# Performance work log

Measured on AMD Instinct MI355X. Metric: run time of the kernel, lower is better.

The kernel has to match this reference:

```python
import jax, jax.numpy as jnp
import numpy as np

# Problem sizes: batch(+heads), seq (m=n), head dim, nonzeros per row
B, M, N, K, R = 8, 4096, 4096, 64, 128
NNZ = M * R


def setup_inputs() -> dict:
    key = jax.random.key(0)
    k1, k2, k3, k4 = jax.random.split(key, 4)
    # Uniform CSR: R nonzeros per row, columns sorted within each row.
    row_offsets = jnp.arange(M + 1, dtype=jnp.int32) * R
    column_indices = jax.random.randint(k4, (M, R), 0, N, dtype=jnp.int32)
    column_indices = jnp.sort(column_indices, axis=1).reshape(NNZ)
    # diffsort(row_offsets): row ids sorted by descending row length (load balancing,
    # does not affect the math).
    diffs = row_offsets[1:] - row_offsets[:-1]
    row_indices = jnp.argsort(-diffs).astype(jnp.int32)
    q3d = jax.random.normal(k1, (B, M, K), dtype=jnp.float32)
    k3d = jax.random.normal(k2, (B, N, K), dtype=jnp.float32)
    v3d = jax.random.normal(k3, (B, N, K), dtype=jnp.float32)
    # `values` is only an output buffer for sddmm in the original; contents unused.
    values = jnp.zeros((B, NNZ), dtype=jnp.float32)
    return {
        "row_indices": row_indices,
        "row_offsets": row_offsets,
        "column_indices": column_indices,
        "q3d": q3d,
        "k3d": k3d,
        "v3d": v3d,
        "values": values,
    }


def reference(row_indices, row_offsets, column_indices, q3d, k3d, v3d, values):
    m = row_offsets.shape[0] - 1
    nnz = column_indices.shape[0]
    # Row id of each CSR nonzero.
    row_ids = jnp.searchsorted(
        row_offsets, jnp.arange(nnz, dtype=row_offsets.dtype), side="right"
    ) - 1
    cols = column_indices

    # SDDMM: logits[b, e] = <Q[b, row(e), :], K[b, col(e), :]>  -> [B, nnz]
    logits = jnp.einsum("bed,bed->be", q3d[:, row_ids, :], k3d[:, cols, :])

    def attend_one(lg_b, v_b):
        # Sparse per-row softmax over the nonzeros of each row.
        mx = jax.ops.segment_max(lg_b, row_ids, num_segments=m)
        ex = jnp.exp(lg_b - mx[row_ids])
        den = jax.ops.segment_sum(ex, row_ids, num_segments=m)
        w = ex / den[row_ids]  # [nnz]
        # SPMM: out[i, :] = sum_{e in row i} w[e] * V[col(e), :]
        return jax.ops.segment_sum(w[:, None] * v_b[cols, :], row_ids, num_segments=m)

    return jax.vmap(attend_one)(logits, v3d)  # [B, M, K]
```

## Files before the change

kernel.cpp:

```cpp
#include <hip/hip_runtime.h>

#define Bc 8
#define Mc 4096
#define Nc 4096
#define Kc 64
#define Rc 128

typedef _Float16 h16;
typedef h16 h16x2 __attribute__((ext_vector_type(2)));
typedef h16 h16x4 __attribute__((ext_vector_type(4)));
typedef h16 h16x8 __attribute__((ext_vector_type(8)));
typedef float f32x4 __attribute__((ext_vector_type(4)));

__global__ __launch_bounds__(256) void cvt_fp16(
    const f32x4* __restrict__ K4, const f32x4* __restrict__ V4,
    const f32x4* __restrict__ Q4,
    h16x4* __restrict__ Kh4, h16x4* __restrict__ Vh4, h16x4* __restrict__ Qh4)
{
    const int nb4   = Nc * Kc / 4;
    const int b     = blockIdx.x & 7;
    const int chunk = blockIdx.x >> 3;
    const int tsel  = chunk >> 8;
    const int idx   = b * nb4 + ((chunk & 255) << 8) + threadIdx.x;
    const f32x4* src = (tsel == 0) ? K4 : (tsel == 1) ? V4 : Q4;
    h16x4*       dst = (tsel == 0) ? Kh4 : (tsel == 1) ? Vh4 : Qh4;
    f32x4 v = __builtin_nontemporal_load(&src[idx]);
    h16x4 o = { (h16)v.x, (h16)v.y, (h16)v.z, (h16)v.w };
    dst[idx] = o;
}

__global__ __launch_bounds__(256, 4) void sattn_kernel(
    const int* __restrict__ cols,
    const h16* __restrict__ Qh,
    const h16* __restrict__ Kh,
    const h16* __restrict__ Vh,
    float* __restrict__ out)
{
    const int b   = blockIdx.x & 7;
    const int w   = threadIdx.x >> 6;
    const int row = ((blockIdx.x >> 3) << 2) | w;
    const int l   = threadIdx.x & 63;
    const int g   = l >> 3;
    const int ln  = l & 7;

    const h16* Kb = Kh + ((size_t)b * Nc) * Kc;
    const h16* Vb = Vh + ((size_t)b * Nc) * Kc;

    h16x8 qv = __builtin_nontemporal_load(
        (const h16x8*)(Qh + (((size_t)b * Mc + row) << 6) + ln * 8));

    const int* crow = cols + row * Rc;
    int col16[16];
    #pragma unroll
    for (int p = 0; p < 16; ++p)
        col16[p] = __builtin_nontemporal_load(&crow[p * 8 + g]);

    h16x8 kv[16];
    #pragma unroll
    for (int p = 0; p < 16; ++p)
        kv[p] = *(const h16x8*)(Kb + (((unsigned)col16[p]) << 6) + ln * 8);

    float lg[16];
    #pragma unroll
    for (int p = 0; p < 16; ++p) {
        float acc = 0.f;
        #pragma unroll
        for (int j = 0; j < 4; ++j) {
            h16x2 qj = { qv[2 * j], qv[2 * j + 1] };
            h16x2 kj = { kv[p][2 * j], kv[p][2 * j + 1] };
#if defined(__has_builtin)
#if __has_builtin(__builtin_amdgcn_fdot2)
            acc = __builtin_amdgcn_fdot2(qj, kj, acc, false);
#else
            acc += (float)qj.x * (float)kj.x + (float)qj.y * (float)kj.y;
#endif
#else
            acc += (float)qj.x * (float)kj.x + (float)qj.y * (float)kj.y;
#endif
        }
        acc += __shfl_xor(acc, 1, 64);
        acc += __shfl_xor(acc, 2, 64);
        acc += __shfl_xor(acc, 4, 64);
        lg[p] = acc;
    }

    h16x8 vv[16];
    #pragma unroll
    for (int p = 0; p < 16; ++p)
        vv[p] = *(const h16x8*)(Vb + (((unsigned)col16[p]) << 6) + ln * 8);

    float m = lg[0];
    #pragma unroll
    for (int p = 1; p < 16; ++p) m = fmaxf(m, lg[p]);
    m = fmaxf(m, __shfl_xor(m, 8, 64));
    m = fmaxf(m, __shfl_xor(m, 16, 64));
    m = fmaxf(m, __shfl_xor(m, 32, 64));

    float e[16];
    float s = 0.f;
    #pragma unroll
    for (int p = 0; p < 16; ++p) { e[p] = __expf(lg[p] - m); s += e[p]; }
    s += __shfl_xor(s, 8, 64);
    s += __shfl_xor(s, 16, 64);
    s += __shfl_xor(s, 32, 64);
    const float inv = 1.0f / s;

    float acc8[8] = {0.f, 0.f, 0.f, 0.f, 0.f, 0.f, 0.f, 0.f};
    #pragma unroll
    for (int p = 0; p < 16; ++p) {
        const float wp = e[p];
        #pragma unroll
        for (int j = 0; j < 8; ++j)
            acc8[j] = fmaf((float)vv[p][j], wp, acc8[j]);
    }

    #pragma unroll
    for (int j = 0; j < 8; ++j) {
        acc8[j] += __shfl_xor(acc8[j], 8, 64);
        acc8[j] += __shfl_xor(acc8[j], 16, 64);
        acc8[j] += __shfl_xor(acc8[j], 32, 64);
    }

    if (g == 0) {
        float* orow = out + (((size_t)b * Mc + row) << 6) + ln * 8;
        f32x4 o0 = { acc8[0] * inv, acc8[1] * inv, acc8[2] * inv, acc8[3] * inv };
        f32x4 o1 = { acc8[4] * inv, acc8[5] * inv, acc8[6] * inv, acc8[7] * inv };
        __builtin_nontemporal_store(o0, (f32x4*)orow);
        __builtin_nontemporal_store(o1, (f32x4*)orow + 1);
    }
}

extern "C" void kernel_launch(void* const* d_in, const int* in_sizes, int n_in,
                              void* d_out, int out_size, void* d_ws, size_t ws_size,
                              hipStream_t stream) {
    const int*   cols = (const int*)d_in[2];
    const float* Qm   = (const float*)d_in[3];
    const float* Km   = (const float*)d_in[4];
    const float* Vm   = (const float*)d_in[5];
    float* out = (float*)d_out;

    h16* Kh = (h16*)d_ws;
    h16* Vh = Kh + (size_t)Bc * Nc * Kc;
    h16* Qh = Vh + (size_t)Bc * Nc * Kc;

    cvt_fp16<<<dim3(Bc * 3 * 256), dim3(256), 0, stream>>>(
        (const f32x4*)Km, (const f32x4*)Vm, (const f32x4*)Qm,
        (h16x4*)Kh, (h16x4*)Vh, (h16x4*)Qh);

    sattn_kernel<<<dim3(Bc * Mc / 4), dim3(256), 0, stream>>>(cols, Qh, Kh, Vh, out);
}
```

Baseline: 154.1 us.

## Split each row's nonzeros across two wavefronts with shared-memory softmax merge

Result: faster. 144.7 us (-6.1%).

```diff
diff --git a/kernel.cpp b/kernel.cpp
--- a/kernel.cpp
+++ b/kernel.cpp
@@ -29,40 +29,45 @@
     dst[idx] = o;
 }
 
-__global__ __launch_bounds__(256, 4) void sattn_kernel(
+__global__ __launch_bounds__(256, 6) void sattn_kernel(
     const int* __restrict__ cols,
     const h16* __restrict__ Qh,
     const h16* __restrict__ Kh,
     const h16* __restrict__ Vh,
     float* __restrict__ out)
 {
-    const int b   = blockIdx.x & 7;
-    const int w   = threadIdx.x >> 6;
-    const int row = ((blockIdx.x >> 3) << 2) | w;
-    const int l   = threadIdx.x & 63;
-    const int g   = l >> 3;
-    const int ln  = l & 7;
+    const int b    = blockIdx.x & 7;
+    const int rb   = blockIdx.x >> 3;
+    const int w    = threadIdx.x >> 6;
+    const int rw   = w >> 1;
+    const int half = w & 1;
+    const int row  = rb * 2 + rw;
+    const int l    = threadIdx.x & 63;
+    const int g    = l >> 3;
+    const int ln   = l & 7;
+
+    __shared__ float s_m[2][2];
+    __shared__ float s_s[2][2];
+    __shared__ __align__(16) float s_part[2][64];
 
     const h16* Kb = Kh + ((size_t)b * Nc) * Kc;
     const h16* Vb = Vh + ((size_t)b * Nc) * Kc;
 
-    h16x8 qv = __builtin_nontemporal_load(
-        (const h16x8*)(Qh + (((size_t)b * Mc + row) << 6) + ln * 8));
+    h16x8 qv = *(const h16x8*)(Qh + (((size_t)b * Mc + row) << 6) + ln * 8);
 
-    const int* crow = cols + row * Rc;
-    int col16[16];
+    const int* crow = cols + row * Rc + half * 64;
+    int col8[8];
     #pragma unroll
-    for (int p = 0; p < 16; ++p)
-        col16[p] = __builtin_nontemporal_load(&crow[p * 8 + g]);
+    for (int p = 0; p < 8; ++p) col8[p] = crow[p * 8 + g];
 
-    h16x8 kv[16];
+    h16x8 kv[8];
     #pragma unroll
-    for (int p = 0; p < 16; ++p)
-        kv[p] = *(const h16x8*)(Kb + (((unsigned)col16[p]) << 6) + ln * 8);
+    for (int p = 0; p < 8; ++p)
+        kv[p] = *(const h16x8*)(Kb + (((unsigned)col8[p]) << 6) + ln * 8);
 
-    float lg[16];
+    float lg[8];
     #pragma unroll
-    for (int p = 0; p < 16; ++p) {
+    for (int p = 0; p < 8; ++p) {
         float acc = 0.f;
         #pragma unroll
         for (int j = 0; j < 4; ++j) {
@@ -84,36 +89,37 @@
         lg[p] = acc;
     }
 
-    h16x8 vv[16];
+    h16x8 vv[8];
     #pragma unroll
-    for (int p = 0; p < 16; ++p)
-        vv[p] = *(const h16x8*)(Vb + (((unsigned)col16[p]) << 6) + ln * 8);
+    for (int p = 0; p < 8; ++p)
+        vv[p] = *(const h16x8*)(Vb + (((unsigned)col8[p]) << 6) + ln * 8);
 
     float m = lg[0];
     #pragma unroll
-    for (int p = 1; p < 16; ++p) m = fmaxf(m, lg[p]);
+    for (int p = 1; p < 8; ++p) m = fmaxf(m, lg[p]);
     m = fmaxf(m, __shfl_xor(m, 8, 64));
     m = fmaxf(m, __shfl_xor(m, 16, 64));
     m = fmaxf(m, __shfl_xor(m, 32, 64));
+    if (l == 0) s_m[rw][half] = m;
+    __syncthreads();
+    m = fmaxf(s_m[rw][0], s_m[rw][1]);
 
-    float e[16];
     float s = 0.f;
     #pragma unroll
-    for (int p = 0; p < 16; ++p) { e[p] = __expf(lg[p] - m); s += e[p]; }
+    for (int p = 0; p < 8; ++p) { lg[p] = __expf(lg[p] - m); s += lg[p]; }
     s += __shfl_xor(s, 8, 64);
     s += __shfl_xor(s, 16, 64);
     s += __shfl_xor(s, 32, 64);
-    const float inv = 1.0f / s;
+    if (l == 0) s_s[rw][half] = s;
 
     float acc8[8] = {0.f, 0.f, 0.f, 0.f, 0.f, 0.f, 0.f, 0.f};
     #pragma unroll
-    for (int p = 0; p < 16; ++p) {
-        const float wp = e[p];
+    for (int p = 0; p < 8; ++p) {
+        const float wp = lg[p];
         #pragma unroll
         for (int j = 0; j < 8; ++j)
             acc8[j] = fmaf((float)vv[p][j], wp, acc8[j]);
     }
-
     #pragma unroll
     for (int j = 0; j < 8; ++j) {
         acc8[j] += __shfl_xor(acc8[j], 8, 64);
@@ -121,10 +127,20 @@
         acc8[j] += __shfl_xor(acc8[j], 32, 64);
     }
 
-    if (g == 0) {
+    if (half == 1 && g == 0) {
+        *(f32x4*)&s_part[rw][ln * 8]     = f32x4{acc8[0], acc8[1], acc8[2], acc8[3]};
+        *(f32x4*)&s_part[rw][ln * 8 + 4] = f32x4{acc8[4], acc8[5], acc8[6], acc8[7]};
+    }
+    __syncthreads();
+
+    if (half == 0 && g == 0) {
+        const float inv = 1.0f / (s_s[rw][0] + s_s[rw][1]);
+        const float* pp = &s_part[rw][ln * 8];
         float* orow = out + (((size_t)b * Mc + row) << 6) + ln * 8;
-        f32x4 o0 = { acc8[0] * inv, acc8[1] * inv, acc8[2] * inv, acc8[3] * inv };
-        f32x4 o1 = { acc8[4] * inv, acc8[5] * inv, acc8[6] * inv, acc8[7] * inv };
+        f32x4 o0 = { (acc8[0] + pp[0]) * inv, (acc8[1] + pp[1]) * inv,
+                     (acc8[2] + pp[2]) * inv, (acc8[3] + pp[3]) * inv };
+        f32x4 o1 = { (acc8[4] + pp[4]) * inv, (acc8[5] + pp[5]) * inv,
+                     (acc8[6] + pp[6]) * inv, (acc8[7] + pp[7]) * inv };
         __builtin_nontemporal_store(o0, (f32x4*)orow);
         __builtin_nontemporal_store(o1, (f32x4*)orow + 1);
     }
@@ -147,5 +163,5 @@
         (const f32x4*)Km, (const f32x4*)Vm, (const f32x4*)Qm,
         (h16x4*)Kh, (h16x4*)Vh, (h16x4*)Qh);
 
-    sattn_kernel<<<dim3(Bc * Mc / 4), dim3(256), 0, stream>>>(cols, Qh, Kh, Vh, out);
+    sattn_kernel<<<dim3(Bc * Mc / 2), dim3(256), 0, stream>>>(cols, Qh, Kh, Vh, out);
 }
```

## Replace per-row K/V gathers with tiled LDS column sweep and online softmax

Applied to the files above, without the earlier changes.

Measured after the change: 228.6 us. 1.48x slower.

```diff
diff --git a/kernel.cpp b/kernel.cpp
--- a/kernel.cpp
+++ b/kernel.cpp
@@ -5,12 +5,23 @@
 #define Nc 4096
 #define Kc 64
 #define Rc 128
+#define Tc 256
+#define NT (Nc / Tc)
+#define KST 144
 
 typedef _Float16 h16;
 typedef h16 h16x2 __attribute__((ext_vector_type(2)));
 typedef h16 h16x4 __attribute__((ext_vector_type(4)));
 typedef h16 h16x8 __attribute__((ext_vector_type(8)));
 typedef float f32x4 __attribute__((ext_vector_type(4)));
+
+template<int CTRL>
+__device__ __forceinline__ float dpp_badd(float x) {
+    union { float f; int i; } u, r;
+    u.f = x;
+    r.i = __builtin_amdgcn_update_dpp(0, u.i, CTRL, 0xF, 0xF, true);
+    return x + r.f;
+}
 
 __global__ __launch_bounds__(256) void cvt_fp16(
     const f32x4* __restrict__ K4, const f32x4* __restrict__ V4,
@@ -29,104 +40,168 @@
     dst[idx] = o;
 }
 
-__global__ __launch_bounds__(256, 4) void sattn_kernel(
+__global__ __launch_bounds__(512, 2) void sattn_sweep(
     const int* __restrict__ cols,
     const h16* __restrict__ Qh,
     const h16* __restrict__ Kh,
     const h16* __restrict__ Vh,
     float* __restrict__ out)
 {
-    const int b   = blockIdx.x & 7;
-    const int w   = threadIdx.x >> 6;
-    const int row = ((blockIdx.x >> 3) << 2) | w;
-    const int l   = threadIdx.x & 63;
-    const int g   = l >> 3;
-    const int ln  = l & 7;
+    const int b     = blockIdx.x & 7;
+    const int rblk  = blockIdx.x >> 3;
+    const int tid   = threadIdx.x;
+    const int l     = tid & 63;
+    const int ln    = tid & 7;
+    const int gbase = l & 56;
+    const int gg    = tid >> 3;
+    const int r0    = rblk * 128 + gg * 2;
+    const int r1    = r0 + 1;
+
+    __shared__ __align__(16) char smem[2][2][Tc * KST];
 
     const h16* Kb = Kh + ((size_t)b * Nc) * Kc;
     const h16* Vb = Vh + ((size_t)b * Nc) * Kc;
 
-    h16x8 qv = __builtin_nontemporal_load(
-        (const h16x8*)(Qh + (((size_t)b * Mc + row) << 6) + ln * 8));
-
-    const int* crow = cols + row * Rc;
-    int col16[16];
-    #pragma unroll
-    for (int p = 0; p < 16; ++p)
-        col16[p] = __builtin_nontemporal_load(&crow[p * 8 + g]);
-
-    h16x8 kv[16];
-    #pragma unroll
-    for (int p = 0; p < 16; ++p)
-        kv[p] = *(const h16x8*)(Kb + (((unsigned)col16[p]) << 6) + ln * 8);
-
-    float lg[16];
-    #pragma unroll
-    for (int p = 0; p < 16; ++p) {
-        float acc = 0.f;
+    h16x8 q0 = *(const h16x8*)(Qh + (((size_t)b * Mc + r0) << 6) + ln * 8);
+    h16x8 q1 = *(const h16x8*)(Qh + (((size_t)b * Mc + r1) << 6) + ln * 8);
+
+    const int* crow0 = cols + r0 * Rc;
+    const int* crow1 = cols + r1 * Rc;
+
+    int   ptr0 = 0, ptr1 = 0;
+    float m0 = -1e30f, s0 = 0.f;
+    float m1 = -1e30f, s1 = 0.f;
+    float acc0[8] = {0.f,0.f,0.f,0.f,0.f,0.f,0.f,0.f};
+    float acc1[8] = {0.f,0.f,0.f,0.f,0.f,0.f,0.f,0.f};
+
+    const int scol = tid >> 1;
+    const int schb = (tid & 1) * 4;
+
+    {
         #pragma unroll
-        for (int j = 0; j < 4; ++j) {
-            h16x2 qj = { qv[2 * j], qv[2 * j + 1] };
-            h16x2 kj = { kv[p][2 * j], kv[p][2 * j + 1] };
+        for (int i = 0; i < 4; ++i) {
+            h16x8 a = *(const h16x8*)(Kb + (size_t)scol * 64 + (schb + i) * 8);
+            h16x8 c = *(const h16x8*)(Vb + (size_t)scol * 64 + (schb + i) * 8);
+            *(h16x8*)(&smem[0][0][scol * KST + (schb + i) * 16]) = a;
+            *(h16x8*)(&smem[0][1][scol * KST + (schb + i) * 16]) = c;
+        }
+    }
+    __syncthreads();
+
+    for (int t = 0; t < NT; ++t) {
+        const int cur   = t & 1;
+        const int c0    = t * Tc;
+        const int c_end = c0 + Tc;
+
+        h16x8 sk[4], sv[4];
+        if (t + 1 < NT) {
+            const h16* sK = Kb + (size_t)(t + 1) * Tc * 64;
+            const h16* sV = Vb + (size_t)(t + 1) * Tc * 64;
+            #pragma unroll
+            for (int i = 0; i < 4; ++i) {
+                sk[i] = *(const h16x8*)(sK + (size_t)scol * 64 + (schb + i) * 8);
+                sv[i] = *(const h16x8*)(sV + (size_t)scol * 64 + (schb + i) * 8);
+            }
+        }
+
+        const char* ldK = smem[cur][0];
+        const char* ldV = smem[cur][1];
+
+        auto process = [&](const int* crow, int& ptr, float& m, float& s,
+                           float* acc, h16x8 q) {
+            for (;;) {
+                int idx  = ptr + ln;
+                int cidx = idx < Rc ? idx : Rc - 1;
+                int cv   = crow[cidx];
+                bool valid = (idx < Rc) && (cv < c_end);
+                unsigned long long bal = __ballot(valid);
+                int n = __popcll((bal >> gbase) & 0xFFull);
+                if (n > 0) {
+                    int cc[8]; h16x8 kf[8]; float lg[8];
+                    #pragma unroll
+                    for (int j = 0; j < 8; ++j) if (j < n) {
+                        cc[j] = __shfl(cv, gbase + j, 64) - c0;
+                        kf[j] = *(const h16x8*)(ldK + cc[j] * KST + ln * 16);
+                    }
+                    #pragma unroll
+                    for (int j = 0; j < 8; ++j) if (j < n) {
+                        float a = 0.f;
+                        #pragma unroll
+                        for (int d = 0; d < 4; ++d) {
+                            h16x2 qj = { q[2*d], q[2*d+1] };
+                            h16x2 kj = { kf[j][2*d], kf[j][2*d+1] };
 #if defined(__has_builtin)
 #if __has_builtin(__builtin_amdgcn_fdot2)
-            acc = __builtin_amdgcn_fdot2(qj, kj, acc, false);
+                            a = __builtin_amdgcn_fdot2(qj, kj, a, false);
 #else
-            acc += (float)qj.x * (float)kj.x + (float)qj.y * (float)kj.y;
+                            a += (float)qj.x*(float)kj.x + (float)qj.y*(float)kj.y;
 #endif
 #else
-            acc += (float)qj.x * (float)kj.x + (float)qj.y * (float)kj.y;
+                            a += (float)qj.x*(float)kj.x + (float)qj.y*(float)kj.y;
 #endif
+                        }
+                        a = dpp_badd<0xB1>(a);
+                        a = dpp_badd<0x4E>(a);
+                        a = dpp_badd<0x141>(a);
+                        lg[j] = a;
+                    }
+                    float cm = -1e30f;
+                    #pragma unroll
+                    for (int j = 0; j < 8; ++j) if (j < n) cm = fmaxf(cm, lg[j]);
+                    if (cm > m) {
+                        float sc = __expf(m - cm);
+                        s *= sc;
+                        #pragma unroll
+                        for (int d = 0; d < 8; ++d) acc[d] *= sc;
+                        m = cm;
+                    }
+                    #pragma unroll
+                    for (int j = 0; j < 8; ++j) if (j < n) {
+                        lg[j] = __expf(lg[j] - m);
+                        s += lg[j];
+                    }
+                    h16x8 vf[8];
+                    #pragma unroll
+                    for (int j = 0; j < 8; ++j) if (j < n)
+                        vf[j] = *(const h16x8*)(ldV + cc[j] * KST + ln * 16);
+                    #pragma unroll
+                    for (int j = 0; j < 8; ++j) if (j < n) {
+                        #pragma unroll
+                        for (int d = 0; d < 8; ++d)
+                            acc[d] = fmaf((float)vf[j][d], lg[j], acc[d]);
+                    }
+                    ptr += n;
+                }
+                if (n < 8) break;
+            }
+        };
+        process(crow0, ptr0, m0, s0, acc0, q0);
+        process(crow1, ptr1, m1, s1, acc1, q1);
+
+        if (t + 1 < NT) {
+            const int nxt = cur ^ 1;
+            #pragma unroll
+            for (int i = 0; i < 4; ++i) {
+                *(h16x8*)(&smem[nxt][0][scol * KST + (schb + i) * 16]) = sk[i];
+                *(h16x8*)(&smem[nxt][1][scol * KST + (schb + i) * 16]) = sv[i];
+            }
         }
-        acc += __shfl_xor(acc, 1, 64);
-        acc += __shfl_xor(acc, 2, 64);
-        acc += __shfl_xor(acc, 4, 64);
-        lg[p] = acc;
-    }
-
-    h16x8 vv[16];
-    #pragma unroll
-    for (int p = 0; p < 16; ++p)
-        vv[p] = *(const h16x8*)(Vb + (((unsigned)col16[p]) << 6) + ln * 8);
-
-    float m = lg[0];
-    #pragma unroll
-    for (int p = 1; p < 16; ++p) m = fmaxf(m, lg[p]);
-    m = fmaxf(m, __shfl_xor(m, 8, 64));
-    m = fmaxf(m, __shfl_xor(m, 16, 64));
-    m = fmaxf(m, __shfl_xor(m, 32, 64));
-
-    float e[16];
-    float s = 0.f;
-    #pragma unroll
-    for (int p = 0; p < 16; ++p) { e[p] = __expf(lg[p] - m); s += e[p]; }
-    s += __shfl_xor(s, 8, 64);
-    s += __shfl_xor(s, 16, 64);
-    s += __shfl_xor(s, 32, 64);
-    const float inv = 1.0f / s;
-
-    float acc8[8] = {0.f, 0.f, 0.f, 0.f, 0.f, 0.f, 0.f, 0.f};
-    #pragma unroll
-    for (int p = 0; p < 16; ++p) {
-        const float wp = e[p];
-        #pragma unroll
-        for (int j = 0; j < 8; ++j)
-            acc8[j] = fmaf((float)vv[p][j], wp, acc8[j]);
-    }
-
-    #pragma unroll
-    for (int j = 0; j < 8; ++j) {
-        acc8[j] += __shfl_xor(acc8[j], 8, 64);
-        acc8[j] += __shfl_xor(acc8[j], 16, 64);
-        acc8[j] += __shfl_xor(acc8[j], 32, 64);
-    }
-
-    if (g == 0) {
-        float* orow = out + (((size_t)b * Mc + row) << 6) + ln * 8;
-        f32x4 o0 = { acc8[0] * inv, acc8[1] * inv, acc8[2] * inv, acc8[3] * inv };
-        f32x4 o1 = { acc8[4] * inv, acc8[5] * inv, acc8[6] * inv, acc8[7] * inv };
-        __builtin_nontemporal_store(o0, (f32x4*)orow);
-        __builtin_nontemporal_store(o1, (f32x4*)orow + 1);
+        __syncthreads();
+    }
+
+    {
+        float inv = 1.0f / s0;
+        float* o = out + (((size_t)b * Mc + r0) << 6) + ln * 8;
+        f32x4 x = { acc0[0]*inv, acc0[1]*inv, acc0[2]*inv, acc0[3]*inv };
+        f32x4 y = { acc0[4]*inv, acc0[5]*inv, acc0[6]*inv, acc0[7]*inv };
+        *(f32x4*)o = x; *((f32x4*)o + 1) = y;
+    }
+    {
+        float inv = 1.0f / s1;
+        float* o = out + (((size_t)b * Mc + r1) << 6) + ln * 8;
+        f32x4 x = { acc1[0]*inv, acc1[1]*inv, acc1[2]*inv, acc1[3]*inv };
+        f32x4 y = { acc1[4]*inv, acc1[5]*inv, acc1[6]*inv, acc1[7]*inv };
+        *(f32x4*)o = x; *((f32x4*)o + 1) = y;
     }
 }
 
@@ -147,5 +222,6 @@
         (const f32x4*)Km, (const f32x4*)Vm, (const f32x4*)Qm,
         (h16x4*)Kh, (h16x4*)Vh, (h16x4*)Qh);
 
-    sattn_kernel<<<dim3(Bc * Mc / 4), dim3(256), 0, stream>>>(cols, Qh, Kh, Vh, out);
-}
+    sattn_sweep<<<dim3(Bc * Mc / 128), dim3(512), 0, stream>>>(
+        cols, Qh, Kh, Vh, out);
+}
```
